# Optimization experiments

Measured on AMD Instinct MI355X. Metric: run time of the kernel, lower is better.

The kernel has to match this reference:

```python
import jax, jax.numpy as jnp
import numpy as np

N = 50000          # nodes
E = 800000         # edges (COO)
IN_CH = 128
H1, H2, OUT = 200, 100, 2   # 100*out, 50*out, out with out_channels=2
EPS = 1e-12
DROP_P = 0.1


def setup_inputs() -> dict:
    key = jax.random.key(0)
    ks = jax.random.split(key, 6)
    x = jax.random.normal(ks[0], (N, IN_CH), dtype=jnp.float32)
    edge_index = jax.random.randint(ks[1], (2, E), 0, N)
    W1 = jax.random.normal(ks[2], (IN_CH, H1), dtype=jnp.float32) / np.sqrt(IN_CH)
    W2 = jax.random.normal(ks[3], (H1, H2), dtype=jnp.float32) / np.sqrt(H1)
    W3 = jax.random.normal(ks[4], (H2, OUT), dtype=jnp.float32) / np.sqrt(H2)
    beta1 = jnp.float32(1.0)
    beta2 = jnp.float32(1.0)
    beta3 = jnp.float32(1.0)
    return dict(x=x, edge_index=edge_index, W1=W1, W2=W2, W3=W3,
                beta1=beta1, beta2=beta2, beta3=beta3)


def _agnn_layer(x, W, beta, src, dst):
    # project in -> out channels, then AGNN cosine-attention propagation
    h = x @ W                                               # [N, D]
    hn = h / jnp.maximum(jnp.linalg.norm(h, axis=-1, keepdims=True), EPS)
    a = beta * jnp.sum(hn[src] * hn[dst], axis=-1)          # [E'] edge logits
    amax = jax.ops.segment_max(a, dst, num_segments=N)      # stable segment softmax
    amax = jnp.where(jnp.isfinite(amax), amax, 0.0)
    e = jnp.exp(a - amax[dst])
    denom = jax.ops.segment_sum(e, dst, num_segments=N)
    alpha = e / jnp.maximum(denom[dst], EPS)
    return jax.ops.segment_sum(h[src] * alpha[:, None], dst, num_segments=N)


def _dropout(k, x, p=DROP_P):
    keep = jax.random.bernoulli(k, 1.0 - p, x.shape)
    return jnp.where(keep, x / (1.0 - p), 0.0)


def reference(x, edge_index, W1, W2, W3, beta1, beta2, beta3):
    src, dst = edge_index[0], edge_index[1]
    loop = jnp.arange(N)                                    # self-loops (AGNNConv default)
    src = jnp.concatenate([src, loop])
    dst = jnp.concatenate([dst, loop])
    k1, k2 = jax.random.split(jax.random.key(42))
    h = jax.nn.relu(_agnn_layer(x, W1, beta1, src, dst))
    h = _dropout(k1, h)
    h = jax.nn.relu(_agnn_layer(h, W2, beta2, src, dst))
    h = _dropout(k2, h)
    h = jax.nn.relu(_agnn_layer(h, W3, beta3, src, dst))
    return h
```

## Files before the change

### kernel.cpp

```cpp
#include <hip/hip_runtime.h>
#include <hip/hip_bf16.h>

#define NN 50000
#define NE 800000
#define EPSN 1e-12f


#define H_OFF    0ull
#define A_OFF    40000000ull
#define H3_OFF   80000000ull
#define RINV_OFF 80400000ull
#define OFFS_OFF 80600000ull
#define DEG_OFF  80800016ull
#define CURS_OFF 81000016ull
#define ESRC_OFF 81200016ull
#define CHNK_OFF 84600016ull

__host__ __device__ inline void tf20(unsigned k0, unsigned k1, unsigned& x0, unsigned& x1) {
  unsigned ks2 = k0 ^ k1 ^ 0x1BD11BDAu;
  x0 += k0; x1 += k1;
#define TFR(r) { x0 += x1; x1 = ((x1 << (r)) | (x1 >> (32 - (r)))) ^ x0; }
  TFR(13) TFR(15) TFR(26) TFR(6)
  x0 += k1;  x1 += ks2 + 1u;
  TFR(17) TFR(29) TFR(16) TFR(24)
  x0 += ks2; x1 += k0 + 2u;
  TFR(13) TFR(15) TFR(26) TFR(6)
  x0 += k0;  x1 += k1 + 3u;
  TFR(17) TFR(29) TFR(16) TFR(24)
  x0 += k1;  x1 += ks2 + 4u;
  TFR(13) TFR(15) TFR(26) TFR(6)
  x0 += ks2; x1 += k0 + 5u;
#undef TFR
}

__device__ __forceinline__ float dropf(float val, unsigned k0, unsigned k1, unsigned i) {
  unsigned x0 = 0u, x1 = i;
  tf20(k0, k1, x0, x1);
  unsigned bits = x0 ^ x1;
  float u = __uint_as_float((bits >> 9) | 0x3F800000u) - 1.0f;
  return (u < 0.9f) ? val * (1.0f / 0.9f) : 0.0f;
}

__device__ __forceinline__ float wave_sum(float x) {
  x += __shfl_xor(x, 32); x += __shfl_xor(x, 16); x += __shfl_xor(x, 8);
  x += __shfl_xor(x, 4);  x += __shfl_xor(x, 2);  x += __shfl_xor(x, 1);
  return x;
}

template<int K, int KT, int NLP, int N>
__device__ __forceinline__ void gemm_core4(float* __restrict__ As, float* __restrict__ Ws,
                                           const float* __restrict__ A,
                                           const float* __restrict__ W,
                                           float* __restrict__ H,
                                           float* __restrict__ RINV, int M, int row0) {
  static_assert(NLP % 64 == 0 && KT % 4 == 0, "layout");
  constexpr int KTP = KT + 1, NV = N / 4, NC = NLP / 64, PD4 = NLP / 4 - NV;
  const float4* A4 = (const float4*)A;
  const float4* W4 = (const float4*)W;
  const float4* Ws4 = (const float4*)Ws;

  int t = threadIdx.x, rgrp = t >> 4, cg = t & 15;
  float acc[4][NC * 4];
#pragma unroll
  for (int rr = 0; rr < 4; rr++)
#pragma unroll
    for (int j = 0; j < NC * 4; j++) acc[rr][j] = 0.f;

  for (int k0 = 0; k0 < K; k0 += KT) {
    __syncthreads();
    for (int idx = t; idx < 64 * (KT / 4); idx += 256) {
      int r = idx / (KT / 4), cq = idx - r * (KT / 4);
      int gr = row0 + r;
      float4 v = (gr < M) ? A4[(size_t)gr * (K / 4) + (k0 / 4) + cq]
                          : make_float4(0.f, 0.f, 0.f, 0.f);
      float* dst = &As[r * KTP + cq * 4];
      dst[0] = v.x; dst[1] = v.y; dst[2] = v.z; dst[3] = v.w;
    }
    for (int idx = t; idx < KT * NV; idx += 256) {
      int kk = idx / NV, cq = idx - kk * NV;
      *(float4*)&Ws[kk * NLP + cq * 4] = W4[(size_t)(k0 + kk) * NV + cq];
    }
    for (int idx = t; idx < KT * PD4; idx += 256) {
      int kk = idx / PD4, pq = idx - kk * PD4;
      *(float4*)&Ws[kk * NLP + N + pq * 4] = make_float4(0.f, 0.f, 0.f, 0.f);
    }
    __syncthreads();
#pragma unroll
    for (int kk = 0; kk < KT; kk++) {
      float a[4];
#pragma unroll
      for (int rr = 0; rr < 4; rr++) a[rr] = As[(rgrp * 4 + rr) * KTP + kk];
#pragma unroll
      for (int q = 0; q < NC; q++) {
        float4 wv = Ws4[kk * (NLP / 4) + cg + 16 * q];
#pragma unroll
        for (int rr = 0; rr < 4; rr++) {
          acc[rr][q * 4 + 0] = fmaf(a[rr], wv.x, acc[rr][q * 4 + 0]);
          acc[rr][q * 4 + 1] = fmaf(a[rr], wv.y, acc[rr][q * 4 + 1]);
          acc[rr][q * 4 + 2] = fmaf(a[rr], wv.z, acc[rr][q * 4 + 2]);
          acc[rr][q * 4 + 3] = fmaf(a[rr], wv.w, acc[rr][q * 4 + 3]);
        }
      }
    }
  }

  int r0 = row0 + rgrp * 4;
#pragma unroll
  for (int rr = 0; rr < 4; rr++) {
    int gr = r0 + rr;
    float ss = 0.f;
#pragma unroll
    for (int q = 0; q < NC; q++) {
#pragma unroll
      for (int j = 0; j < 4; j++) {
        float v = acc[rr][q * 4 + j];
        ss += v * v;
        int c = 4 * (cg + 16 * q) + j;
        if (gr < M && c < N) H[(size_t)gr * N + c] = v;
      }
    }
    ss += __shfl_xor(ss, 1); ss += __shfl_xor(ss, 2);
    ss += __shfl_xor(ss, 4); ss += __shfl_xor(ss, 8);
    if (cg == 0 && gr < M) RINV[gr] = 1.0f / fmaxf(sqrtf(ss), EPSN);
  }
}

__global__ __launch_bounds__(256, 4) void gemm1_hist_kernel(
    const float* __restrict__ X, const float* __restrict__ W1,
    float* __restrict__ H, float* __restrict__ RINV,
    const int* __restrict__ EI, int* __restrict__ DEG) {
  __shared__ float As[64 * 17];
  __shared__ float Ws[16 * 256];
  int bid = blockIdx.x;
  if (bid < 782) {
    gemm_core4<128, 16, 256, 200>(As, Ws, X, W1, H, RINV, NN, bid * 64);
  } else {
    for (int e = (bid - 782) * 256 + threadIdx.x; e < NE; e += 242 * 256)
      atomicAdd(&DEG[EI[NE + e]], 1);
  }
}

__global__ __launch_bounds__(256, 4) void gemm2_kernel(const float* __restrict__ A,
                                                       const float* __restrict__ W,
                                                       float* __restrict__ H,
                                                       float* __restrict__ RINV, int M) {
  __shared__ float As[64 * 41];
  __shared__ float Ws[40 * 128];
  gemm_core4<200, 40, 128, 100>(As, Ws, A, W, H, RINV, M, blockIdx.x * 64);
}

__global__ __launch_bounds__(256) void csr_scan1_kernel(const int* __restrict__ deg,
                                                        int* __restrict__ offs,
                                                        int* __restrict__ chunk) {
  __shared__ int lds[8];
  int t = threadIdx.x;
  int base = blockIdx.x * 1024 + t * 4;
  int d[4];
#pragma unroll
  for (int j = 0; j < 4; j++) d[j] = (base + j < NN) ? deg[base + j] : 0;
  int ts = d[0] + d[1] + d[2] + d[3];
  int lane = t & 63, wave = t >> 6;
  int inc = ts;
#pragma unroll
  for (int sh = 1; sh < 64; sh <<= 1) { int u = __shfl_up(inc, sh); if (lane >= sh) inc += u; }
  if (lane == 63) lds[wave] = inc;
  __syncthreads();
  if (t == 0) { int s = 0; for (int w = 0; w < 4; w++) { int x = lds[w]; lds[w] = s; s += x; } lds[4] = s; }
  __syncthreads();
  int p = lds[wave] + inc - ts;
#pragma unroll
  for (int j = 0; j < 4; j++) { if (base + j < NN) offs[base + j] = p; p += d[j]; }
  if (t == 255) chunk[blockIdx.x] = lds[4];
}

__global__ __launch_bounds__(64) void csr_scan2_kernel(int* __restrict__ chunk) {
  int t = threadIdx.x;
  int v = (t < 49) ? chunk[t] : 0;
  int inc = v;
#pragma unroll
  for (int sh = 1; sh < 64; sh <<= 1) { int u = __shfl_up(inc, sh); if (t >= sh) inc += u; }
  if (t < 49) chunk[t] = inc - v;
}

__global__ __launch_bounds__(256) void csr_scan3_kernel(int* __restrict__ offs,
                                                        const int* __restrict__ chunk,
                                                        int* __restrict__ curs) {
  int i = blockIdx.x * 256 + threadIdx.x;
  if (i < NN) {
    int val = offs[i] + chunk[i >> 10];
    offs[i] = val;
    curs[i] = val;
  }
  if (i == 0) offs[NN] = NE;
}

__global__ __launch_bounds__(256) void csr_scatter_kernel(const int* __restrict__ ei,
                                                          int* __restrict__ curs,
                                                          int* __restrict__ esrc) {
  int e = blockIdx.x * 256 + threadIdx.x;
  if (e >= NE) return;
  int s = ei[e], d = ei[NE + e];
  int pos = atomicAdd(&curs[d], 1);
  esrc[pos] = s;
}

template<int D, int VEC, bool DROP>
__device__ __forceinline__ void attn_body(const float* __restrict__ H,
                                          const float* __restrict__ RINV,
                                          const int* __restrict__ OFFS,
                                          const int* __restrict__ ESRC,
                                          const float* __restrict__ BETA,
                                          float* __restrict__ OUT,
                                          unsigned k0, unsigned k1) {
  constexpr int NL = D / VEC;
  int v = blockIdx.x * 4 + (threadIdx.x >> 6);
  int lane = threadIdx.x & 63;
  bool act = lane < NL;
  float beta = BETA[0];
  float bd = beta * RINV[v];
  int e0 = OFFS[v], e1 = OFFS[v + 1];

  float wself = __expf(beta);
  float s = wself;
  float hd[VEC], acc[VEC];
  if (act) {
    const float* hrow = H + (size_t)v * D + lane * VEC;
    if (VEC == 4) { float4 tv = *(const float4*)hrow; hd[0] = tv.x; hd[1] = tv.y; hd[2] = tv.z; hd[3] = tv.w; }
    else          { float2 tv = *(const float2*)hrow; hd[0] = tv.x; hd[1] = tv.y; }
#pragma unroll
    for (int j = 0; j < VEC; j++) acc[j] = wself * hd[j];
  }

  int idx = e0;
  for (; idx + 4 <= e1; idx += 4) {
    int   u[4];
    float r[4], dt[4], hs[4][VEC];
#pragma unroll
    for (int m = 0; m < 4; m++) u[m] = ESRC[idx + m];
#pragma unroll
    for (int m = 0; m < 4; m++) r[m] = RINV[u[m]];
    float dd[4] = {0.f, 0.f, 0.f, 0.f};
    if (act) {
#pragma unroll
      for (int m = 0; m < 4; m++) {
        const float* p = H + (size_t)u[m] * D + lane * VEC;
        if (VEC == 4) { float4 a = *(const float4*)p; hs[m][0] = a.x; hs[m][1] = a.y; hs[m][2] = a.z; hs[m][3] = a.w; }
        else          { float2 a = *(const float2*)p; hs[m][0] = a.x; hs[m][1] = a.y; }
      }
#pragma unroll
      for (int m = 0; m < 4; m++)
#pragma unroll
        for (int j = 0; j < VEC; j++) dd[m] = fmaf(hd[j], hs[m][j], dd[m]);
    }
#pragma unroll
    for (int m = 0; m < 4; m++) dt[m] = wave_sum(dd[m]);
    float w[4];
#pragma unroll
    for (int m = 0; m < 4; m++) { w[m] = __expf(bd * dt[m] * r[m]); s += w[m]; }
    if (act) {
#pragma unroll
      for (int m = 0; m < 4; m++)
#pragma unroll
        for (int j = 0; j < VEC; j++) acc[j] = fmaf(w[m], hs[m][j], acc[j]);
    }
  }
  for (; idx < e1; ++idx) {
    int u0 = ESRC[idx];
    float r0 = RINV[u0];
    float h0[VEC];
    float ddt = 0.f;
    if (act) {
      const float* p0 = H + (size_t)u0 * D + lane * VEC;
      if (VEC == 4) { float4 a = *(const float4*)p0; h0[0] = a.x; h0[1] = a.y; h0[2] = a.z; h0[3] = a.w; }
      else          { float2 a = *(const float2*)p0; h0[0] = a.x; h0[1] = a.y; }
#pragma unroll
      for (int j = 0; j < VEC; j++) ddt = fmaf(hd[j], h0[j], ddt);
    }
    ddt = wave_sum(ddt);
    float w0 = __expf(bd * ddt * r0);
    s += w0;
    if (act) {
#pragma unroll
      for (int j = 0; j < VEC; j++) acc[j] = fmaf(w0, h0[j], acc[j]);
    }
  }

  float rs = 1.0f / fmaxf(s, EPSN);
  if (act) {
    float o[VEC];
#pragma unroll
    for (int j = 0; j < VEC; j++) {
      float val = acc[j] * rs;
      val = (val <= 0.0f) ? 0.0f : val;
      if (DROP) val = dropf(val, k0, k1, (unsigned)(v * D + lane * VEC + j));
      o[j] = val;
    }
    float* orow = OUT + (size_t)v * D + lane * VEC;
    if (VEC == 4) *(float4*)orow = make_float4(o[0], o[1], o[2], o[3]);
    else          *(float2*)orow = make_float2(o[0], o[1]);
  }
}

__global__ __launch_bounds__(256) void attn1_kernel(const float* H, const float* RINV,
                                                    const int* OFFS, const int* ESRC,
                                                    const float* BETA, float* OUT,
                                                    unsigned k0, unsigned k1) {
  attn_body<200, 4, true>(H, RINV, OFFS, ESRC, BETA, OUT, k0, k1);
}
__global__ __launch_bounds__(256) void attn2_kernel(const float* H, const float* RINV,
                                                    const int* OFFS, const int* ESRC,
                                                    const float* BETA, float* OUT,
                                                    unsigned k0, unsigned k1) {
  attn_body<100, 2, true>(H, RINV, OFFS, ESRC, BETA, OUT, k0, k1);
}

__global__ __launch_bounds__(256) void gemm3_kernel(const float* __restrict__ A2,
                                                    const float* __restrict__ W3,
                                                    float* __restrict__ H3,
                                                    float* __restrict__ RINV) {
  __shared__ float w3s[200];
  for (int i = threadIdx.x; i < 200; i += 256) w3s[i] = W3[i];
  __syncthreads();
  int v = blockIdx.x * 256 + threadIdx.x;
  if (v >= NN) return;
  const float* row = A2 + (size_t)v * 100;
  float o0 = 0.f, o1 = 0.f;
#pragma unroll 4
  for (int k = 0; k < 100; k++) {
    float x = row[k];
    o0 = fmaf(x, w3s[2 * k], o0);
    o1 = fmaf(x, w3s[2 * k + 1], o1);
  }
  H3[2 * v] = o0; H3[2 * v + 1] = o1;
  RINV[v] = 1.0f / fmaxf(sqrtf(o0 * o0 + o1 * o1), EPSN);
}

__global__ __launch_bounds__(256) void attn3_kernel(const float* __restrict__ H3,
                                                    const float* __restrict__ RINV,
                                                    const int* __restrict__ OFFS,
                                                    const int* __restrict__ ESRC,
                                                    const float* __restrict__ BETA,
                                                    float* __restrict__ out) {
  int v = blockIdx.x * 4 + (threadIdx.x >> 6);
  int lane = threadIdx.x & 63;
  float beta = BETA[0];
  float bd = beta * RINV[v];
  float h0 = H3[2 * v], h1 = H3[2 * v + 1];
  int e0 = OFFS[v], e1 = OFFS[v + 1];
  float s = 0.f, a0 = 0.f, a1 = 0.f;
  for (int idx = e0 + lane; idx < e1; idx += 64) {
    int u = ESRC[idx];
    float s0 = H3[2 * u], s1 = H3[2 * u + 1];
    float w = __expf(bd * (h0 * s0 + h1 * s1) * RINV[u]);
    s += w; a0 = fmaf(w, s0, a0); a1 = fmaf(w, s1, a1);
  }
  s = wave_sum(s); a0 = wave_sum(a0); a1 = wave_sum(a1);
  if (lane == 0) {
    float wself = __expf(beta);
    s += wself; a0 = fmaf(wself, h0, a0); a1 = fmaf(wself, h1, a1);
    float rs = 1.0f / fmaxf(s, EPSN);
    float o0 = a0 * rs, o1 = a1 * rs;
    out[2 * v]     = (o0 <= 0.0f) ? 0.0f : o0;
    out[2 * v + 1] = (o1 <= 0.0f) ? 0.0f : o1;
  }
}

extern "C" void kernel_launch(void* const* d_in, const int* in_sizes, int n_in,
                              void* d_out, int out_size, void* d_ws, size_t ws_size,
                              hipStream_t stream) {
  const float* X  = (const float*)d_in[0];
  const int*   EI = (const int*)d_in[1];
  const float* W1 = (const float*)d_in[2];
  const float* W2 = (const float*)d_in[3];
  const float* W3 = (const float*)d_in[4];
  const float* B1 = (const float*)d_in[5];
  const float* B2 = (const float*)d_in[6];
  const float* B3 = (const float*)d_in[7];

  char* ws = (char*)d_ws;
  float* H    = (float*)(ws + H_OFF);
  float* A    = (float*)(ws + A_OFF);
  float* H3   = (float*)(ws + H3_OFF);
  float* RINV = (float*)(ws + RINV_OFF);
  int* OFFS   = (int*)(ws + OFFS_OFF);
  int* DEG    = (int*)(ws + DEG_OFF);
  int* CURS   = (int*)(ws + CURS_OFF);
  int* ESRC   = (int*)(ws + ESRC_OFF);
  int* CHNK   = (int*)(ws + CHNK_OFF);

  unsigned k1a = 0u, k1b = 0u; tf20(0u, 42u, k1a, k1b);
  unsigned k2a = 0u, k2b = 1u; tf20(0u, 42u, k2a, k2b);

  hipMemsetAsync(DEG, 0, NN * sizeof(int), stream);

  gemm1_hist_kernel<<<1024, 256, 0, stream>>>(X, W1, H, RINV, EI, DEG);
  csr_scan1_kernel<<<49, 256, 0, stream>>>(DEG, OFFS, CHNK);
  csr_scan2_kernel<<<1, 64, 0, stream>>>(CHNK);
  csr_scan3_kernel<<<196, 256, 0, stream>>>(OFFS, CHNK, CURS);
  csr_scatter_kernel<<<(NE + 255) / 256, 256, 0, stream>>>(EI, CURS, ESRC);

  const int gb = (NN + 63) / 64;
  const int ab = NN / 4;

  attn1_kernel<<<ab, 256, 0, stream>>>(H, RINV, OFFS, ESRC, B1, A, k1a, k1b);
  gemm2_kernel<<<gb, 256, 0, stream>>>(A, W2, H, RINV, NN);
  attn2_kernel<<<ab, 256, 0, stream>>>(H, RINV, OFFS, ESRC, B2, A, k2a, k2b);
  gemm3_kernel<<<(NN + 255) / 256, 256, 0, stream>>>(A, W3, H3, RINV);
  attn3_kernel<<<ab, 256, 0, stream>>>(H3, RINV, OFFS, ESRC, B3, (float*)d_out);
}
```

Baseline: 472.1 us.

## Split GEMM1 to overlap CSR scatter, fuse layer-3 projection into attn2

The first GEMM is split into two halves. One half runs alongside the degree histogram and the other alongside the CSR scatter, so the scatter kernel is no longer a standalone serial launch. The attn2 kernel now applies dropout and then projects each output row through W3 with a wave reduction, writing H3 and its inverse norms directly. This removes the separate gemm3 pass and the write and reread of the 100-wide layer-2 activations. RINV3 reuses the CURS buffer, which is dead after the scatter, and the projection adds two extra wave reductions per node.

```diff
diff --git a/kernel.cpp b/kernel.cpp
--- a/kernel.cpp
+++ b/kernel.cpp
@@ -125,18 +125,37 @@
   }
 }
 
-__global__ __launch_bounds__(256, 4) void gemm1_hist_kernel(
+__global__ __launch_bounds__(256, 4) void gemm1a_hist_kernel(
     const float* __restrict__ X, const float* __restrict__ W1,
     float* __restrict__ H, float* __restrict__ RINV,
     const int* __restrict__ EI, int* __restrict__ DEG) {
   __shared__ float As[64 * 17];
   __shared__ float Ws[16 * 256];
   int bid = blockIdx.x;
-  if (bid < 782) {
+  if (bid < 391) {
     gemm_core4<128, 16, 256, 200>(As, Ws, X, W1, H, RINV, NN, bid * 64);
   } else {
-    for (int e = (bid - 782) * 256 + threadIdx.x; e < NE; e += 242 * 256)
+    for (int e = (bid - 391) * 256 + threadIdx.x; e < NE; e += 242 * 256)
       atomicAdd(&DEG[EI[NE + e]], 1);
+  }
+}
+
+__global__ __launch_bounds__(256, 4) void gemm1b_scat_kernel(
+    const float* __restrict__ X, const float* __restrict__ W1,
+    float* __restrict__ H, float* __restrict__ RINV,
+    const int* __restrict__ EI, int* __restrict__ CURS,
+    int* __restrict__ ESRC) {
+  __shared__ float As[64 * 17];
+  __shared__ float Ws[16 * 256];
+  int bid = blockIdx.x;
+  if (bid < 391) {
+    gemm_core4<128, 16, 256, 200>(As, Ws, X, W1, H, RINV, NN, (bid + 391) * 64);
+  } else {
+    for (int e = (bid - 391) * 256 + threadIdx.x; e < NE; e += 242 * 256) {
+      int s = EI[e], d = EI[NE + e];
+      int pos = atomicAdd(&CURS[d], 1);
+      ESRC[pos] = s;
+    }
   }
 }
 
@@ -192,16 +211,6 @@
     curs[i] = val;
   }
   if (i == 0) offs[NN] = NE;
-}
-
-__global__ __launch_bounds__(256) void csr_scatter_kernel(const int* __restrict__ ei,
-                                                          int* __restrict__ curs,
-                                                          int* __restrict__ esrc) {
-  int e = blockIdx.x * 256 + threadIdx.x;
-  if (e >= NE) return;
-  int s = ei[e], d = ei[NE + e];
-  int pos = atomicAdd(&curs[d], 1);
-  esrc[pos] = s;
 }
 
 template<int D, int VEC, bool DROP>
@@ -307,36 +316,110 @@
                                                     unsigned k0, unsigned k1) {
   attn_body<200, 4, true>(H, RINV, OFFS, ESRC, BETA, OUT, k0, k1);
 }
-__global__ __launch_bounds__(256) void attn2_kernel(const float* H, const float* RINV,
-                                                    const int* OFFS, const int* ESRC,
-                                                    const float* BETA, float* OUT,
-                                                    unsigned k0, unsigned k1) {
-  attn_body<100, 2, true>(H, RINV, OFFS, ESRC, BETA, OUT, k0, k1);
-}
-
-__global__ __launch_bounds__(256) void gemm3_kernel(const float* __restrict__ A2,
-                                                    const float* __restrict__ W3,
-                                                    float* __restrict__ H3,
-                                                    float* __restrict__ RINV) {
-  __shared__ float w3s[200];
-  for (int i = threadIdx.x; i < 200; i += 256) w3s[i] = W3[i];
-  __syncthreads();
-  int v = blockIdx.x * 256 + threadIdx.x;
-  if (v >= NN) return;
-  const float* row = A2 + (size_t)v * 100;
-  float o0 = 0.f, o1 = 0.f;
-#pragma unroll 4
-  for (int k = 0; k < 100; k++) {
-    float x = row[k];
-    o0 = fmaf(x, w3s[2 * k], o0);
-    o1 = fmaf(x, w3s[2 * k + 1], o1);
-  }
-  H3[2 * v] = o0; H3[2 * v + 1] = o1;
-  RINV[v] = 1.0f / fmaxf(sqrtf(o0 * o0 + o1 * o1), EPSN);
+
+__global__ __launch_bounds__(256) void attn2_proj_kernel(
+    const float* __restrict__ H, const float* __restrict__ RINV,
+    const int* __restrict__ OFFS, const int* __restrict__ ESRC,
+    const float* __restrict__ BETA, const float* __restrict__ W3,
+    float* __restrict__ H3, float* __restrict__ RINV3,
+    unsigned k0, unsigned k1) {
+  constexpr int D = 100, VEC = 2, NL = 50;
+  int v = blockIdx.x * 4 + (threadIdx.x >> 6);
+  int lane = threadIdx.x & 63;
+  bool act = lane < NL;
+  float beta = BETA[0];
+  float bd = beta * RINV[v];
+  int e0 = OFFS[v], e1 = OFFS[v + 1];
+
+  float4 w3v = make_float4(0.f, 0.f, 0.f, 0.f);
+  if (act) w3v = *(const float4*)&W3[4 * lane];
+
+  float wself = __expf(beta);
+  float s = wself;
+  float hd[VEC], acc[VEC];
+  if (act) {
+    const float* hrow = H + (size_t)v * D + lane * VEC;
+    float2 tv = *(const float2*)hrow; hd[0] = tv.x; hd[1] = tv.y;
+#pragma unroll
+    for (int j = 0; j < VEC; j++) acc[j] = wself * hd[j];
+  }
+
+  int idx = e0;
+  for (; idx + 4 <= e1; idx += 4) {
+    int   u[4];
+    float r[4], dt[4], hs[4][VEC];
+#pragma unroll
+    for (int m = 0; m < 4; m++) u[m] = ESRC[idx + m];
+#pragma unroll
+    for (int m = 0; m < 4; m++) r[m] = RINV[u[m]];
+    float dd[4] = {0.f, 0.f, 0.f, 0.f};
+    if (act) {
+#pragma unroll
+      for (int m = 0; m < 4; m++) {
+        const float* p = H + (size_t)u[m] * D + lane * VEC;
+        float2 a = *(const float2*)p; hs[m][0] = a.x; hs[m][1] = a.y;
+      }
+#pragma unroll
+      for (int m = 0; m < 4; m++)
+#pragma unroll
+        for (int j = 0; j < VEC; j++) dd[m] = fmaf(hd[j], hs[m][j], dd[m]);
+    }
+#pragma unroll
+    for (int m = 0; m < 4; m++) dt[m] = wave_sum(dd[m]);
+    float w[4];
+#pragma unroll
+    for (int m = 0; m < 4; m++) { w[m] = __expf(bd * dt[m] * r[m]); s += w[m]; }
+    if (act) {
+#pragma unroll
+      for (int m = 0; m < 4; m++)
+#pragma unroll
+        for (int j = 0; j < VEC; j++) acc[j] = fmaf(w[m], hs[m][j], acc[j]);
+    }
+  }
+  for (; idx < e1; ++idx) {
+    int u0 = ESRC[idx];
+    float r0 = RINV[u0];
+    float h0[VEC];
+    float ddt = 0.f;
+    if (act) {
+      const float* p0 = H + (size_t)u0 * D + lane * VEC;
+      float2 a = *(const float2*)p0; h0[0] = a.x; h0[1] = a.y;
+#pragma unroll
+      for (int j = 0; j < VEC; j++) ddt = fmaf(hd[j], h0[j], ddt);
+    }
+    ddt = wave_sum(ddt);
+    float w0 = __expf(bd * ddt * r0);
+    s += w0;
+    if (act) {
+#pragma unroll
+      for (int j = 0; j < VEC; j++) acc[j] = fmaf(w0, h0[j], acc[j]);
+    }
+  }
+
+  float rs = 1.0f / fmaxf(s, EPSN);
+  float p0 = 0.f, p1 = 0.f;
+  if (act) {
+    float o[VEC];
+#pragma unroll
+    for (int j = 0; j < VEC; j++) {
+      float val = acc[j] * rs;
+      val = (val <= 0.0f) ? 0.0f : val;
+      val = dropf(val, k0, k1, (unsigned)(v * D + lane * VEC + j));
+      o[j] = val;
+    }
+    p0 = o[0] * w3v.x + o[1] * w3v.z;
+    p1 = o[0] * w3v.y + o[1] * w3v.w;
+  }
+  p0 = wave_sum(p0);
+  p1 = wave_sum(p1);
+  if (lane == 0) {
+    H3[2 * v] = p0; H3[2 * v + 1] = p1;
+    RINV3[v] = 1.0f / fmaxf(sqrtf(p0 * p0 + p1 * p1), EPSN);
+  }
 }
 
 __global__ __launch_bounds__(256) void attn3_kernel(const float* __restrict__ H3,
-                                                    const float* __restrict__ RINV,
+                                                    const float* __restrict__ RINV3,
                                                     const int* __restrict__ OFFS,
                                                     const int* __restrict__ ESRC,
                                                     const float* __restrict__ BETA,
@@ -344,14 +427,14 @@
   int v = blockIdx.x * 4 + (threadIdx.x >> 6);
   int lane = threadIdx.x & 63;
   float beta = BETA[0];
-  float bd = beta * RINV[v];
+  float bd = beta * RINV3[v];
   float h0 = H3[2 * v], h1 = H3[2 * v + 1];
   int e0 = OFFS[v], e1 = OFFS[v + 1];
   float s = 0.f, a0 = 0.f, a1 = 0.f;
   for (int idx = e0 + lane; idx < e1; idx += 64) {
     int u = ESRC[idx];
     float s0 = H3[2 * u], s1 = H3[2 * u + 1];
-    float w = __expf(bd * (h0 * s0 + h1 * s1) * RINV[u]);
+    float w = __expf(bd * (h0 * s0 + h1 * s1) * RINV3[u]);
     s += w; a0 = fmaf(w, s0, a0); a1 = fmaf(w, s1, a1);
   }
   s = wave_sum(s); a0 = wave_sum(a0); a1 = wave_sum(a1);
@@ -378,33 +461,33 @@
   const float* B3 = (const float*)d_in[7];
 
   char* ws = (char*)d_ws;
-  float* H    = (float*)(ws + H_OFF);
-  float* A    = (float*)(ws + A_OFF);
-  float* H3   = (float*)(ws + H3_OFF);
-  float* RINV = (float*)(ws + RINV_OFF);
-  int* OFFS   = (int*)(ws + OFFS_OFF);
-  int* DEG    = (int*)(ws + DEG_OFF);
-  int* CURS   = (int*)(ws + CURS_OFF);
-  int* ESRC   = (int*)(ws + ESRC_OFF);
-  int* CHNK   = (int*)(ws + CHNK_OFF);
+  float* H     = (float*)(ws + H_OFF);
+  float* A     = (float*)(ws + A_OFF);
+  float* H3    = (float*)(ws + H3_OFF);
+  float* RINV  = (float*)(ws + RINV_OFF);
+  int* OFFS    = (int*)(ws + OFFS_OFF);
+  int* DEG     = (int*)(ws + DEG_OFF);
+  int* CURS    = (int*)(ws + CURS_OFF);
+  float* RINV3 = (float*)(ws + CURS_OFF);
+  int* ESRC    = (int*)(ws + ESRC_OFF);
+  int* CHNK    = (int*)(ws + CHNK_OFF);
 
   unsigned k1a = 0u, k1b = 0u; tf20(0u, 42u, k1a, k1b);
   unsigned k2a = 0u, k2b = 1u; tf20(0u, 42u, k2a, k2b);
 
   hipMemsetAsync(DEG, 0, NN * sizeof(int), stream);
 
-  gemm1_hist_kernel<<<1024, 256, 0, stream>>>(X, W1, H, RINV, EI, DEG);
+  gemm1a_hist_kernel<<<633, 256, 0, stream>>>(X, W1, H, RINV, EI, DEG);
   csr_scan1_kernel<<<49, 256, 0, stream>>>(DEG, OFFS, CHNK);
   csr_scan2_kernel<<<1, 64, 0, stream>>>(CHNK);
   csr_scan3_kernel<<<196, 256, 0, stream>>>(OFFS, CHNK, CURS);
-  csr_scatter_kernel<<<(NE + 255) / 256, 256, 0, stream>>>(EI, CURS, ESRC);
+  gemm1b_scat_kernel<<<633, 256, 0, stream>>>(X, W1, H, RINV, EI, CURS, ESRC);
 
   const int gb = (NN + 63) / 64;
   const int ab = NN / 4;
 
   attn1_kernel<<<ab, 256, 0, stream>>>(H, RINV, OFFS, ESRC, B1, A, k1a, k1b);
   gemm2_kernel<<<gb, 256, 0, stream>>>(A, W2, H, RINV, NN);
-  attn2_kernel<<<ab, 256, 0, stream>>>(H, RINV, OFFS, ESRC, B2, A, k2a, k2b);
-  gemm3_kernel<<<(NN + 255) / 256, 256, 0, stream>>>(A, W3, H3, RINV);
-  attn3_kernel<<<ab, 256, 0, stream>>>(H3, RINV, OFFS, ESRC, B3, (float*)d_out);
-}
+  attn2_proj_kernel<<<ab, 256, 0, stream>>>(H, RINV, OFFS, ESRC, B2, W3, H3, RINV3, k2a, k2b);
+  attn3_kernel<<<ab, 256, 0, stream>>>(H3, RINV3, OFFS, ESRC, B3, (float*)d_out);
+}
```

Result: slower. 488.3 us (+3.4%).
